# Kernel tuning notes

Measured on AMD Instinct MI355X. Metric: run time of the kernel, lower is better.

The kernel has to match this reference:

```python
import jax, jax.numpy as jnp
import numpy as np

NUM_NODES = 94
SEQ_LEN = 784
OUT_CLASSES = 10
ALPHA = 0.5
GAMMA = 0.1
OMEGA = 2.0 * np.pi / 28.0
H = 1.0
INV_SQRT_N = 1.0 / np.sqrt(NUM_NODES)


def _xavier(key, shape):
    fan_in, fan_out = shape[1], shape[0]
    limit = np.sqrt(6.0 / (fan_in + fan_out))
    return jax.random.uniform(key, shape, jnp.float32, -limit, limit)


def setup_inputs() -> dict:
    key = jax.random.key(0)
    k_in, k_ih, k_hh, k_ro = jax.random.split(key, 4)
    batch = 1024
    return {
        "input_sequence": jax.random.normal(k_in, (batch, SEQ_LEN), jnp.float32),
        "w_ih": _xavier(k_ih, (NUM_NODES, 1)),   # Linear(1 -> N) weight
        "b_ih": jnp.zeros((NUM_NODES,), jnp.float32),
        "w_hh": _xavier(k_hh, (NUM_NODES, NUM_NODES)),  # Linear(N -> N) weight
        "b_hh": jnp.zeros((NUM_NODES,), jnp.float32),
        "w_ro": _xavier(k_ro, (OUT_CLASSES, NUM_NODES)),  # readout weight
        "b_ro": jnp.zeros((OUT_CLASSES,), jnp.float32),
    }


def reference(input_sequence, w_ih, b_ih, w_hh, b_hh, w_ro, b_ro):
    batch = input_sequence.shape[0]
    # precompute external drive for all steps: [T, B, N]
    # W_ih(s_t) with input_dim=1 is an outer product: s_t * w_ih[:,0] + b_ih
    s = input_sequence.T  # [T, B]
    w_ih_vec = w_ih[:, 0]  # [N]

    def step(carry, s_t):
        x, y = carry
        I_ext = s_t[:, None] * w_ih_vec[None, :] + b_ih  # [B, N]
        I_rec = y @ w_hh.T + b_hh                        # [B, N]
        A = (I_ext + I_rec) * INV_SQRT_N
        accel = ALPHA * jnp.tanh(A) - 2.0 * GAMMA * y - (OMEGA ** 2) * x
        x_new = x + H * y
        y_new = y + H * accel
        return (x_new, y_new), None

    x0 = jnp.zeros((batch, NUM_NODES), jnp.float32)
    y0 = jnp.zeros((batch, NUM_NODES), jnp.float32)
    (x_final, _), _ = jax.lax.scan(step, (x0, y0), s)
    return x_final @ w_ro.T + b_ro  # [B, 10]
```

## Files before the change

kernel.cpp:

```cpp
#include <hip/hip_runtime.h>
#include <math.h>

#define NUM_NODES 94
#define SEQ_LEN 784
#define OUT_CLASSES 10
#define EPB 16
#define NW 6
#define SP 788
#define YHALF 1664

#define TWO_GAMMA 0.2f
#define OM2 0.0503551324598949f
#define INV_SQRT_N 0.103142124625879
#define LOG2E 1.4426950408889634
#define WSCALE ((float)(2.0 * INV_SQRT_N * LOG2E))

typedef _Float16 half8 __attribute__((ext_vector_type(8)));
typedef _Float16 half4 __attribute__((ext_vector_type(4)));
typedef _Float16 half2v __attribute__((ext_vector_type(2)));
typedef float    floatx4 __attribute__((ext_vector_type(4)));
typedef float    f2 __attribute__((ext_vector_type(2)));

__global__
__attribute__((amdgpu_flat_work_group_size(NW*64, NW*64)))
void horn_kernel(
    const float* __restrict__ input,
    const float* __restrict__ w_ih,
    const float* __restrict__ b_ih,
    const float* __restrict__ w_hh,
    const float* __restrict__ b_hh,
    const float* __restrict__ w_ro,
    const float* __restrict__ b_ro,
    float* __restrict__ out)
{
    __shared__ __align__(16) float    sinl[EPB * SP];
    __shared__ __align__(16) _Float16 ybuf[2][YHALF];

    const int tid  = threadIdx.x;
    const int w    = tid >> 6;
    const int lane = tid & 63;
    const int e    = lane & 15;
    const int h    = lane >> 4;
    const int bb   = blockIdx.x;

    const int  T        = w;
    const bool duty     = (w == 3 && h == 0);
    const bool tailmask = (w == 5 && h == 3);

    const int eoff = 104 * e + 4 * (e >> 3);

    {
        const floatx4* in4 = (const floatx4*)(input + (size_t)bb * EPB * SEQ_LEN);
        for (int idx = tid; idx < EPB * (SEQ_LEN / 4); idx += NW * 64) {
            int ee = idx / (SEQ_LEN / 4);
            int cc = idx - ee * (SEQ_LEN / 4);
            *(floatx4*)&sinl[ee * SP + 4 * cc] = in4[ee * (SEQ_LEN / 4) + cc];
        }
    }
    for (int i = tid; i < (2 * YHALF) / 2; i += NW * 64) ((float*)ybuf)[i] = 0.0f;

    const int arow = 16 * T + e;
    half8 a0, a1, a2;
    #pragma unroll
    for (int i = 0; i < 8; ++i) {
        const int k = 8 * h + i;
        float v0 = 0.0f, v1 = 0.0f, v2 = 0.0f;
        if (arow < NUM_NODES) {
            v0 = w_hh[arow * NUM_NODES + k] * WSCALE;
            if (k + 32 < NUM_NODES) v1 = w_hh[arow * NUM_NODES + k + 32] * WSCALE;
            const int k2 = k + 64;
            if      (k2 <  NUM_NODES) v2 = w_hh[arow * NUM_NODES + k2] * WSCALE;
            else if (k2 == NUM_NODES) v2 = w_ih[arow] * WSCALE;
            else                      v2 = (b_ih[arow] + b_hh[arow]) * WSCALE;
        }
        a0[i] = (_Float16)v0; a1[i] = (_Float16)v1; a2[i] = (_Float16)v2;
    }

    f2 x01 = {0,0}, x23 = {0,0}, y01 = {0,0}, y23 = {0,0};

    const floatx4 zf4 = {0,0,0,0};
    const f2 no2 = {-OM2, -OM2};
    const f2 p82 = {1.0f - TWO_GAMMA, 1.0f - TWO_GAMMA};
    const f2 h05 = {0.5f, 0.5f};

    __syncthreads();

    if (tid < EPB) {
        const int eo = 104 * tid + 4 * (tid >> 3);
        const float s0 = input[((size_t)bb * EPB + tid) * SEQ_LEN];
        half2v v0; v0[0] = (_Float16)s0; v0[1] = (_Float16)1.0f;
        half2v v1; v1[0] = (_Float16)0.0f; v1[1] = (_Float16)1.0f;
        *(half2v*)&ybuf[0][eo + NUM_NODES] = v0;
        *(half2v*)&ybuf[1][eo + NUM_NODES] = v1;
    }
    __syncthreads();

    #define HSTEP(RP, WP, T_) do {                                                 \
        const _Float16* Yb = &ybuf[RP][eoff + 8 * h];                              \
        half4 l0 = *(const half4*)(Yb);                                            \
        half4 u0 = *(const half4*)(Yb + 4);                                        \
        half4 l1 = *(const half4*)(Yb + 32);                                       \
        half4 u1 = *(const half4*)(Yb + 36);                                       \
        half4 l2 = *(const half4*)(Yb + 64);                                       \
        half4 u2 = *(const half4*)(Yb + 68);                                       \
                                \
        f2 q01 = no2 * x01 + h05;  q01 = p82 * y01 + q01;                          \
        f2 q23 = no2 * x23 + h05;  q23 = p82 * y23 + q23;                          \
        x01 += y01;  x23 += y23;                                                   \
        float snext = 0.0f;                                                        \
        if (duty) {                                                                \
            const int tn = ((T_) + 1 < SEQ_LEN) ? (T_) + 1 : (SEQ_LEN - 1);        \
            snext = sinl[e * SP + tn];                                             \
        }                                                                          \
        half8 B0 = __builtin_shufflevector(l0, u0, 0, 1, 2, 3, 4, 5, 6, 7);        \
        half8 B1 = __builtin_shufflevector(l1, u1, 0, 1, 2, 3, 4, 5, 6, 7);        \
        half8 B2 = __builtin_shufflevector(l2, u2, 0, 1, 2, 3, 4, 5, 6, 7);        \
        floatx4 d0 = __builtin_amdgcn_mfma_f32_16x16x32_f16(a0, B0, zf4, 0, 0, 0); \
        floatx4 d1 = __builtin_amdgcn_mfma_f32_16x16x32_f16(a1, B1, zf4, 0, 0, 0); \
        floatx4 d2 = __builtin_amdgcn_mfma_f32_16x16x32_f16(a2, B2, zf4, 0, 0, 0); \
        floatx4 d = (d0 + d1) + d2;    \
        f2 r01, r23;                                                               \
        r01[0] = __builtin_amdgcn_rcpf(__builtin_amdgcn_exp2f(d[0]) + 1.0f);       \
        r01[1] = __builtin_amdgcn_rcpf(__builtin_amdgcn_exp2f(d[1]) + 1.0f);       \
        r23[0] = __builtin_amdgcn_rcpf(__builtin_amdgcn_exp2f(d[2]) + 1.0f);       \
        r23[1] = __builtin_amdgcn_rcpf(__builtin_amdgcn_exp2f(d[3]) + 1.0f);       \
        y01 = q01 - r01;  y23 = q23 - r23;                                         \
        half4 yh;                                                                  \
        yh[0] = (_Float16)y01[0]; yh[1] = (_Float16)y01[1];                        \
        yh[2] = (_Float16)y23[0]; yh[3] = (_Float16)y23[1];                        \
        if (tailmask) {                                                            \
            half2v yt; yt[0] = yh[0]; yt[1] = yh[1];          \
            *(half2v*)&ybuf[WP][eoff + 92] = yt;                                   \
        } else {                                                                   \
            *(half4*)&ybuf[WP][eoff + 16 * T + 4 * h] = yh;                        \
        }                                                                          \
        if (duty) {                                                                \
            half2v sv; sv[0] = (_Float16)snext; sv[1] = (_Float16)1.0f;            \
            *(half2v*)&ybuf[WP][eoff + NUM_NODES] = sv;                            \
        }                                                                          \
        __syncthreads();                                                           \
    } while (0)

    for (int t = 0; t < SEQ_LEN; t += 2) {
        HSTEP(0, 1, t);
        HSTEP(1, 0, t + 1);
    }
    #undef HSTEP

    float* xsh = sinl;
    {
        floatx4 xv;
        xv[0] = x01[0]; xv[1] = x01[1]; xv[2] = x23[0]; xv[3] = x23[1];
        *(floatx4*)&xsh[e * 104 + 16 * T + 4 * h] = xv;
    }
    __syncthreads();

    if (tid < EPB * OUT_CLASSES) {
        const int ee = tid / OUT_CLASSES;
        const int c  = tid - ee * OUT_CLASSES;
        float acc = b_ro[c];
        #pragma unroll 2
        for (int r = 0; r < NUM_NODES; ++r)
            acc += xsh[ee * 104 + r] * w_ro[c * NUM_NODES + r];
        out[((size_t)bb * EPB + ee) * OUT_CLASSES + c] = acc;
    }
}

extern "C" void kernel_launch(void* const* d_in, const int* in_sizes, int n_in,
                              void* d_out, int out_size, void* d_ws, size_t ws_size,
                              hipStream_t stream) {
    const float* input = (const float*)d_in[0];
    const float* w_ih  = (const float*)d_in[1];
    const float* b_ih  = (const float*)d_in[2];
    const float* w_hh  = (const float*)d_in[3];
    const float* b_hh  = (const float*)d_in[4];
    const float* w_ro  = (const float*)d_in[5];
    const float* b_ro  = (const float*)d_in[6];
    float* out = (float*)d_out;

    const int batch = in_sizes[0] / SEQ_LEN;
    dim3 grid(batch / EPB);
    dim3 block(NW * 64);

    hipLaunchKernelGGL(horn_kernel, grid, block, 0, stream,
                       input, w_ih, b_ih, w_hh, b_hh, w_ro, b_ro, out);
}
```

Before: 303.4 us.

## Split last two row tiles across extra waves to shorten per-step latency

After: 298.3 us. Within noise of the previous version (-1.7%).

```diff
diff --git a/kernel.cpp b/kernel.cpp
--- a/kernel.cpp
+++ b/kernel.cpp
@@ -5,9 +5,9 @@
 #define SEQ_LEN 784
 #define OUT_CLASSES 10
 #define EPB 16
-#define NW 6
+#define NW 8
 #define SP 788
-#define YHALF 1664
+#define YP 104
 
 #define TWO_GAMMA 0.2f
 #define OM2 0.0503551324598949f
@@ -34,7 +34,7 @@
     float* __restrict__ out)
 {
     __shared__ __align__(16) float    sinl[EPB * SP];
-    __shared__ __align__(16) _Float16 ybuf[2][YHALF];
+    __shared__ __align__(16) _Float16 ybuf[2][EPB * YP];
 
     const int tid  = threadIdx.x;
     const int w    = tid >> 6;
@@ -43,9 +43,10 @@
     const int h    = lane >> 4;
     const int bb   = blockIdx.x;
 
-    const int  T        = w;
-    const bool duty     = (w == 3 && h == 0);
-    const bool tailmask = (w == 5 && h == 3);
+    const bool isfull = (w < 4);
+    const int  T      = isfull ? w : (4 + ((w - 4) >> 1));
+    const int  p      = (w - 4) & 1;
+    const bool duty   = (w == 7) && (h == 3);
 
     const int eoff = 104 * e + 4 * (e >> 3);
 
@@ -54,89 +55,97 @@
         for (int idx = tid; idx < EPB * (SEQ_LEN / 4); idx += NW * 64) {
             int ee = idx / (SEQ_LEN / 4);
             int cc = idx - ee * (SEQ_LEN / 4);
-            *(floatx4*)&sinl[ee * SP + 4 * cc] = in4[ee * (SEQ_LEN / 4) + cc];
+            *(floatx4*)&sinl[ee * SP + 4 * cc] = in4[idx];
         }
     }
-    for (int i = tid; i < (2 * YHALF) / 2; i += NW * 64) ((float*)ybuf)[i] = 0.0f;
+    for (int i = tid; i < (2 * EPB * YP) / 2; i += NW * 64) ((float*)ybuf)[i] = 0.0f;
+    __syncthreads();
+    if (tid < EPB) {
+        const int eo = 104 * tid + 4 * (tid >> 3);
+        const float s0 = sinl[tid * SP];
+        half2v v; v[0] = (_Float16)s0; v[1] = (_Float16)1.0f;
+        *(half2v*)&ybuf[0][eo + NUM_NODES] = v;
+    }
+    __syncthreads();
 
     const int arow = 16 * T + e;
-    half8 a0, a1, a2;
+    half8 A0, A1, A2;
     #pragma unroll
     for (int i = 0; i < 8; ++i) {
         const int k = 8 * h + i;
         float v0 = 0.0f, v1 = 0.0f, v2 = 0.0f;
         if (arow < NUM_NODES) {
             v0 = w_hh[arow * NUM_NODES + k] * WSCALE;
-            if (k + 32 < NUM_NODES) v1 = w_hh[arow * NUM_NODES + k + 32] * WSCALE;
+            v1 = w_hh[arow * NUM_NODES + k + 32] * WSCALE;
             const int k2 = k + 64;
             if      (k2 <  NUM_NODES) v2 = w_hh[arow * NUM_NODES + k2] * WSCALE;
             else if (k2 == NUM_NODES) v2 = w_ih[arow] * WSCALE;
             else                      v2 = (b_ih[arow] + b_hh[arow]) * WSCALE;
         }
-        a0[i] = (_Float16)v0; a1[i] = (_Float16)v1; a2[i] = (_Float16)v2;
+        A0[i] = (_Float16)v0; A1[i] = (_Float16)v1; A2[i] = (_Float16)v2;
     }
 
     f2 x01 = {0,0}, x23 = {0,0}, y01 = {0,0}, y23 = {0,0};
 
-    const floatx4 zf4 = {0,0,0,0};
     const f2 no2 = {-OM2, -OM2};
     const f2 p82 = {1.0f - TWO_GAMMA, 1.0f - TWO_GAMMA};
     const f2 h05 = {0.5f, 0.5f};
-
-    __syncthreads();
-
-    if (tid < EPB) {
-        const int eo = 104 * tid + 4 * (tid >> 3);
-        const float s0 = input[((size_t)bb * EPB + tid) * SEQ_LEN];
-        half2v v0; v0[0] = (_Float16)s0; v0[1] = (_Float16)1.0f;
-        half2v v1; v1[0] = (_Float16)0.0f; v1[1] = (_Float16)1.0f;
-        *(half2v*)&ybuf[0][eo + NUM_NODES] = v0;
-        *(half2v*)&ybuf[1][eo + NUM_NODES] = v1;
-    }
-    __syncthreads();
+    const floatx4 zf4 = {0,0,0,0};
 
     #define HSTEP(RP, WP, T_) do {                                                 \
-        const _Float16* Yb = &ybuf[RP][eoff + 8 * h];                              \
-        half4 l0 = *(const half4*)(Yb);                                            \
-        half4 u0 = *(const half4*)(Yb + 4);                                        \
-        half4 l1 = *(const half4*)(Yb + 32);                                       \
-        half4 u1 = *(const half4*)(Yb + 36);                                       \
-        half4 l2 = *(const half4*)(Yb + 64);                                       \
-        half4 u2 = *(const half4*)(Yb + 68);                                       \
-                                \
-        f2 q01 = no2 * x01 + h05;  q01 = p82 * y01 + q01;                          \
-        f2 q23 = no2 * x23 + h05;  q23 = p82 * y23 + q23;                          \
-        x01 += y01;  x23 += y23;                                                   \
-        float snext = 0.0f;                                                        \
+        const _Float16* yb = &ybuf[RP][eoff + 8 * h];                              \
+        half4 l0 = *(const half4*)(yb);                                            \
+        half4 u0 = *(const half4*)(yb + 4);                                        \
+        half4 l1 = *(const half4*)(yb + 32);                                       \
+        half4 u1 = *(const half4*)(yb + 36);                                       \
+        half4 l2 = *(const half4*)(yb + 64);                                       \
+        half4 u2 = *(const half4*)(yb + 68);                                       \
+        float sn = 0.0f;                                                           \
         if (duty) {                                                                \
             const int tn = ((T_) + 1 < SEQ_LEN) ? (T_) + 1 : (SEQ_LEN - 1);        \
-            snext = sinl[e * SP + tn];                                             \
+            sn = sinl[e * SP + tn];                                                \
+        }                                                                          \
+                         \
+        f2 q0 = no2 * x01 + h05;  q0 = p82 * y01 + q0;                             \
+        x01 += y01;                                                                \
+        f2 q1 = {0.0f, 0.0f};                                                      \
+        if (isfull) {                                                              \
+            q1 = no2 * x23 + h05;  q1 = p82 * y23 + q1;                            \
+            x23 += y23;                                                            \
         }                                                                          \
         half8 B0 = __builtin_shufflevector(l0, u0, 0, 1, 2, 3, 4, 5, 6, 7);        \
         half8 B1 = __builtin_shufflevector(l1, u1, 0, 1, 2, 3, 4, 5, 6, 7);        \
         half8 B2 = __builtin_shufflevector(l2, u2, 0, 1, 2, 3, 4, 5, 6, 7);        \
-        floatx4 d0 = __builtin_amdgcn_mfma_f32_16x16x32_f16(a0, B0, zf4, 0, 0, 0); \
-        floatx4 d1 = __builtin_amdgcn_mfma_f32_16x16x32_f16(a1, B1, zf4, 0, 0, 0); \
-        floatx4 d2 = __builtin_amdgcn_mfma_f32_16x16x32_f16(a2, B2, zf4, 0, 0, 0); \
-        floatx4 d = (d0 + d1) + d2;    \
-        f2 r01, r23;                                                               \
-        r01[0] = __builtin_amdgcn_rcpf(__builtin_amdgcn_exp2f(d[0]) + 1.0f);       \
-        r01[1] = __builtin_amdgcn_rcpf(__builtin_amdgcn_exp2f(d[1]) + 1.0f);       \
-        r23[0] = __builtin_amdgcn_rcpf(__builtin_amdgcn_exp2f(d[2]) + 1.0f);       \
-        r23[1] = __builtin_amdgcn_rcpf(__builtin_amdgcn_exp2f(d[3]) + 1.0f);       \
-        y01 = q01 - r01;  y23 = q23 - r23;                                         \
-        half4 yh;                                                                  \
-        yh[0] = (_Float16)y01[0]; yh[1] = (_Float16)y01[1];                        \
-        yh[2] = (_Float16)y23[0]; yh[3] = (_Float16)y23[1];                        \
-        if (tailmask) {                                                            \
-            half2v yt; yt[0] = yh[0]; yt[1] = yh[1];          \
-            *(half2v*)&ybuf[WP][eoff + 92] = yt;                                   \
+        floatx4 d0 = __builtin_amdgcn_mfma_f32_16x16x32_f16(A0, B0, zf4, 0, 0, 0); \
+        floatx4 d1 = __builtin_amdgcn_mfma_f32_16x16x32_f16(A1, B1, zf4, 0, 0, 0); \
+        floatx4 d2 = __builtin_amdgcn_mfma_f32_16x16x32_f16(A2, B2, zf4, 0, 0, 0); \
+        floatx4 d = (d0 + d1) + d2;      \
+        if (isfull) {                                                              \
+            f2 r0, r1;                                                             \
+            r0[0] = __builtin_amdgcn_rcpf(__builtin_amdgcn_exp2f(d[0]) + 1.0f);    \
+            r0[1] = __builtin_amdgcn_rcpf(__builtin_amdgcn_exp2f(d[1]) + 1.0f);    \
+            r1[0] = __builtin_amdgcn_rcpf(__builtin_amdgcn_exp2f(d[2]) + 1.0f);    \
+            r1[1] = __builtin_amdgcn_rcpf(__builtin_amdgcn_exp2f(d[3]) + 1.0f);    \
+            y01 = q0 - r0;  y23 = q1 - r1;                                         \
+            half4 yh;                                                              \
+            yh[0] = (_Float16)y01[0]; yh[1] = (_Float16)y01[1];                    \
+            yh[2] = (_Float16)y23[0]; yh[3] = (_Float16)y23[1];                    \
+            *(half4*)&ybuf[WP][eoff + 16 * T + 4 * h] = yh;                        \
         } else {                                                                   \
-            *(half4*)&ybuf[WP][eoff + 16 * T + 4 * h] = yh;                        \
-        }                                                                          \
-        if (duty) {                                                                \
-            half2v sv; sv[0] = (_Float16)snext; sv[1] = (_Float16)1.0f;            \
-            *(half2v*)&ybuf[WP][eoff + NUM_NODES] = sv;                            \
+            f2 dv;                                                                 \
+            if (p == 0) { dv[0] = d[0]; dv[1] = d[1]; }                            \
+            else        { dv[0] = d[2]; dv[1] = d[3]; }                            \
+            f2 r;                                                                  \
+            r[0] = __builtin_amdgcn_rcpf(__builtin_amdgcn_exp2f(dv[0]) + 1.0f);    \
+            r[1] = __builtin_amdgcn_rcpf(__builtin_amdgcn_exp2f(dv[1]) + 1.0f);    \
+            y01 = q0 - r;                                                          \
+            if (duty) {                                                            \
+                half2v sv; sv[0] = (_Float16)sn; sv[1] = (_Float16)1.0f;           \
+                *(half2v*)&ybuf[WP][eoff + NUM_NODES] = sv;                        \
+            } else {                                                               \
+                half2v yh2; yh2[0] = (_Float16)y01[0]; yh2[1] = (_Float16)y01[1];  \
+                *(half2v*)&ybuf[WP][eoff + 16 * T + 4 * h + 2 * p] = yh2;          \
+            }                                                                      \
         }                                                                          \
         __syncthreads();                                                           \
     } while (0)
@@ -148,10 +157,13 @@
     #undef HSTEP
 
     float* xsh = sinl;
-    {
+    if (isfull) {
         floatx4 xv;
         xv[0] = x01[0]; xv[1] = x01[1]; xv[2] = x23[0]; xv[3] = x23[1];
-        *(floatx4*)&xsh[e * 104 + 16 * T + 4 * h] = xv;
+        *(floatx4*)&xsh[e * 100 + 16 * T + 4 * h] = xv;
+    } else {
+        f2 xv; xv[0] = x01[0]; xv[1] = x01[1];
+        *(f2*)&xsh[e * 100 + 16 * T + 4 * h + 2 * p] = xv;
     }
     __syncthreads();
 
@@ -161,7 +173,7 @@
         float acc = b_ro[c];
         #pragma unroll 2
         for (int r = 0; r < NUM_NODES; ++r)
-            acc += xsh[ee * 104 + r] * w_ro[c * NUM_NODES + r];
+            acc += xsh[ee * 100 + r] * w_ro[c * NUM_NODES + r];
         out[((size_t)bb * EPB + ee) * OUT_CLASSES + c] = acc;
     }
 }
```
